# Kernel optimization log

Hardware: AMD Instinct MI355X
Metric: run time of the kernel (lower is better)

The kernel has to match this reference:

```python
import jax, jax.numpy as jnp
import numpy as np

N_QUBITS = 8
DEPTH = 6
BATCH = 32
C = jnp.complex64

# Noise strengths from get_ibm_noise_params: constants derived from IBM Nairobi gate errors.
G1, G2 = 0.0003, 0.0065

def _amp_kraus(g):
    return [jnp.array([[1.0, 0.0], [0.0, np.sqrt(1.0 - g)]], C),
            jnp.array([[0.0, np.sqrt(g)], [0.0, 0.0]], C)]

def _phase_kraus(g):
    return [jnp.array([[1.0, 0.0], [0.0, np.sqrt(1.0 - g)]], C),
            jnp.array([[0.0, 0.0], [0.0, np.sqrt(g)]], C)]

def _depol_kraus(p):
    s0, s = np.sqrt(1.0 - p), np.sqrt(p / 3.0)
    I = np.eye(2); X = np.array([[0, 1], [1, 0]])
    Y = np.array([[0, -1j], [1j, 0]]); Z = np.diag([1, -1])
    return [jnp.array(s0 * I, C), jnp.array(s * X, C), jnp.array(s * Y, C), jnp.array(s * Z, C)]

# channels applied sequentially: amplitude damping, phase damping, depolarizing
CH_1Q = [_amp_kraus(G1 * 0.3), _phase_kraus(G1 * 0.2), _depol_kraus(G1 * 0.5)]
CH_2Q = [_amp_kraus(G2 * 0.3), _phase_kraus(G2 * 0.2), _depol_kraus(G2 * 0.5)]

CNOT4 = jnp.array([[1, 0, 0, 0], [0, 1, 0, 0], [0, 0, 0, 1], [0, 0, 1, 0]], C).reshape(2, 2, 2, 2)

# rho is a per-sample tensor of shape (2,)*(2*N): axes [0..N) are row indices, [N..2N) col indices.

def apply_1q(rho, U, w):
    # rho -> U rho U^dagger on wire w
    rho = jnp.moveaxis(jnp.tensordot(U, rho, axes=([1], [w])), 0, w)
    return jnp.moveaxis(jnp.tensordot(jnp.conj(U), rho, axes=([1], [N_QUBITS + w])), 0, N_QUBITS + w)

def apply_channel(rho, kraus, w):
    out = apply_1q(rho, kraus[0], w)
    for K in kraus[1:]:
        out = out + apply_1q(rho, K, w)
    return out

def apply_noise(rho, channels, w):
    for kraus in channels:
        rho = apply_channel(rho, kraus, w)
    return rho

def apply_cnot(rho, w):
    rho = jnp.moveaxis(jnp.tensordot(CNOT4, rho, axes=([2, 3], [w, w + 1])), [0, 1], [w, w + 1])
    return jnp.moveaxis(jnp.tensordot(jnp.conj(CNOT4), rho,
                                      axes=([2, 3], [N_QUBITS + w, N_QUBITS + w + 1])),
                        [0, 1], [N_QUBITS + w, N_QUBITS + w + 1])

def ry(t):
    c, s = jnp.cos(t / 2), jnp.sin(t / 2)
    return jnp.stack([jnp.stack([c, -s]), jnp.stack([s, c])]).astype(C)

def rz(t):
    em = jnp.exp(-0.5j * t).astype(C)  # exp(-i t/2)
    zero = jnp.zeros((), C)
    return jnp.stack([jnp.stack([em, zero]), jnp.stack([zero, jnp.conj(em)])])

def circuit(x, weights):
    # x: [N_QUBITS] angles; weights: [DEPTH, N_QUBITS, 2]
    shape = (2,) * (2 * N_QUBITS)
    rho = jnp.zeros(shape, C).at[(0,) * (2 * N_QUBITS)].set(1.0)

    def encode(rho, x):
        for i in range(N_QUBITS):
            rho = apply_1q(rho, ry(x[i]), i)
            rho = apply_noise(rho, CH_1Q, i)
        return rho

    rho = jax.checkpoint(encode)(rho, x)

    def layer(rho, wl):
        for i in range(N_QUBITS - 1):
            rho = apply_cnot(rho, i)
            rho = apply_noise(rho, CH_2Q, i)
            rho = apply_noise(rho, CH_2Q, i + 1)
        for i in range(N_QUBITS):
            rho = apply_1q(rho, ry(wl[i, 0]), i)
            rho = apply_1q(rho, rz(wl[i, 1]), i)
            rho = apply_noise(rho, CH_1Q, i)
        return rho, None

    rho, _ = jax.lax.scan(jax.checkpoint(layer), rho, weights)

    D = 2 ** N_QUBITS
    diag = jnp.diagonal(rho.reshape(D, D))
    # PauliZ on wire 0 (most significant bit in PennyLane ordering): +1 first half, -1 second half
    sign = jnp.where(jnp.arange(D) < D // 2, 1.0, -1.0)
    return jnp.real(jnp.sum(diag * sign)).astype(jnp.float32)


def setup_inputs() -> dict:
    key = jax.random.key(0)
    k1, k2 = jax.random.split(key)
    x = jax.random.normal(k1, (BATCH, N_QUBITS), dtype=jnp.float32)
    weights = jax.random.normal(k2, (DEPTH, N_QUBITS, 2), dtype=jnp.float32) * 0.1
    return {"x": x, "weights": weights}


def reference(x, weights):
    out = jax.vmap(circuit, in_axes=(0, None))(x, weights)  # [B]
    return out[:, None]  # [B, 1], matches torch .unsqueeze(1)
```

## Files before the change

### kernel.cpp

```cpp
#include <hip/hip_runtime.h>
#include <cmath>


typedef float2 cplx;
#define BATCH 32

__device__ __forceinline__ cplx cmul(cplx a, cplx b){
  return make_float2(a.x*b.x - a.y*b.y, a.x*b.y + a.y*b.x);
}
__device__ __forceinline__ cplx lc(float a, cplx u, float b, cplx v){
  return make_float2(a*u.x + b*v.x, a*u.y + b*v.y);
}
__device__ __forceinline__ cplx sc(float a, cplx u){ return make_float2(a*u.x, a*u.y); }

struct N1C { float A,B,C,D,E; };
__device__ __forceinline__ N1C noise_coeffs(float g){
  float ga = g*0.3f, gp = g*0.2f, p = g*0.5f;
  N1C n;
  n.A = 1.0f - 2.0f*p/3.0f;
  n.D = 2.0f*p/3.0f;
  n.B = ga*n.A + n.D*(1.0f-ga);
  n.E = n.D*ga + n.A*(1.0f-ga);
  n.C = (1.0f - 4.0f*p/3.0f) * sqrtf(1.0f-ga) * sqrtf(1.0f-gp);
  return n;
}
__device__ __forceinline__ N1C mkadj(N1C n){
  N1C a; a.A=n.A; a.B=n.D; a.C=n.C; a.D=n.B; a.E=n.E; return a;
}

__device__ __forceinline__ int physof(int L){
  int rl = L >> 6;
  int rot = ((rl<<3)|(rl>>3)) & 63;
  return L ^ rot;
}
__device__ __forceinline__ constexpr int KPc(int p){
  return (p < 6) ? (1<<p) : ((1<<p) | (1 << ((p-3)%6)));
}
__device__ __forceinline__ int physB(int L){
  int rl = L >> 5;
  int rot = ((rl<<2)|(rl>>3)) & 31;
  return L ^ rot;
}
__device__ __forceinline__ constexpr int maskB(int p){
  return (p < 5) ? (1<<p) : ((1<<p) | (1 << ((p-3)%5)));
}

template<int U>
__device__ __forceinline__ int baseF(int g){
  constexpr int F[6][8] = {
    {0,0,0,0,0,0,0,0},
    {2,4,9, 3,5,8,10,11},
    {0,3,5, 4,6,9,10,11},
    {0,1,4, 5,6,7,10,11},
    {1,2,5, 0,6,7,8,11},
    {0,2,3, 1,6,7,8,9}};
  int b = 0;
  #pragma unroll
  for (int i=0;i<8;i++) b ^= (-((g>>i)&1)) & KPc(F[U][i]);
  return b;
}
template<int V>
__device__ __forceinline__ int baseBk(int g){
  constexpr int F[5][6] = {
    {0,0,0,0,0,0},
    {3,4, 2,7,8,9},
    {0,4, 3,5,8,9},
    {0,1, 4,5,6,9},
    {1,2, 0,5,6,7}};
  int b = 0;
  #pragma unroll
  for (int i=0;i<6;i++) b ^= (-((g>>i)&1)) & maskB(F[V][i]);
  return b;
}
__device__ __forceinline__ int base_s(int t){
  constexpr int P[10] = {1,2,3,9, 4,5,7,8,10,11};
  int b = 0;
  #pragma unroll
  for (int i=0;i<10;i++) b ^= (-((t>>i)&1)) & KPc(P[i]);
  return b;
}

__device__ __forceinline__ void rot_pair(cplx& v0, cplx& v1, float cy, float sy){
  cplx a=v0, b=v1;
  v0 = make_float2(cy*a.x - sy*b.x, cy*a.y - sy*b.y);
  v1 = make_float2(sy*a.x + cy*b.x, sy*a.y + cy*b.y);
}

template<int U>
__device__ __forceinline__ void fstage2(cplx* __restrict__ slab, float4 rc, int bp, int bsel,
                                        N1C n1, N1C n2, float a0, float b0, float a1, float b1){
  constexpr int KA=KPc(6+U), KB=KPc(5+U), KC=1<<U, KD=1<<(U-1);
  cplx h[8];
  #pragma unroll
  for (int i=0;i<8;i++){
    int a=(i>>2)&1, cc=(i>>1)&1, d=i&1;
    h[i] = slab[bp ^ (a?KA:0) ^ ((bsel^a)?KB:0) ^ (cc?KC:0) ^ ((d^cc)?KD:0)];
  }
  #pragma unroll
  for (int d=0;d<2;d++){
    cplx t00=h[d], t11=h[6|d];
    h[d]   = lc(n2.A,t00, n2.B,t11);
    h[6|d] = lc(n2.D,t00, n2.E,t11);
    h[2|d] = sc(n2.C, h[2|d]);
    h[4|d] = sc(n2.C, h[4|d]);
  }
  #pragma unroll
  for (int j=0;j<4;j++){
    int i0 = j<<1;
    float r0x = __shfl_xor(h[i0].x, 1, 64),   r0y = __shfl_xor(h[i0].y, 1, 64);
    float r1x = __shfl_xor(h[i0|1].x, 1, 64), r1y = __shfl_xor(h[i0|1].y, 1, 64);
    cplx h0 = h[i0], h1 = h[i0|1];
    h[i0]   = make_float2(a0*h0.x + b0*r1x, a0*h0.y + b0*r1y);
    h[i0|1] = make_float2(a1*h1.x + b1*r0x, a1*h1.y + b1*r0y);
  }
  float cy=rc.x, sy=rc.y;
  #pragma unroll
  for (int a=0;a<2;a++)
    #pragma unroll
    for (int d=0;d<2;d++) rot_pair(h[(a<<2)|d], h[(a<<2)|2|d], cy, sy);
  #pragma unroll
  for (int cc=0;cc<2;cc++)
    #pragma unroll
    for (int d=0;d<2;d++) rot_pair(h[(cc<<1)|d], h[4|(cc<<1)|d], cy, sy);
  cplx p = make_float2(rc.z, rc.w), pcj = make_float2(rc.z, -rc.w);
  #pragma unroll
  for (int d=0;d<2;d++){
    cplx t00=h[d], t11=h[6|d];
    h[d]   = lc(n1.A,t00, n1.B,t11);
    h[6|d] = lc(n1.D,t00, n1.E,t11);
    h[2|d] = cmul(p,   h[2|d]);
    h[4|d] = cmul(pcj, h[4|d]);
  }
  #pragma unroll
  for (int i=0;i<8;i++){
    int a=(i>>2)&1, cc=(i>>1)&1, d=i&1;
    slab[bp ^ (a?KA:0) ^ (bsel?KB:0) ^ (cc?KC:0) ^ (d?KD:0)] = h[i];
  }
}

__device__ __forceinline__ void redT50(cplx* __restrict__ slab, float4 rc, float g6,
                                       N1C n1, N1C n2, int t){
  constexpr int KR = KPc(6), KCb = 1;
  #pragma unroll
  for (int grp=0; grp<2; grp++){
    int bp = base_s(t | (grp<<9));
    cplx v00 = slab[bp], v01 = slab[bp^KCb], v10 = slab[bp^KR], v11 = slab[bp^KR^KCb];
    v01 = sc(g6, v01); v10 = sc(g6, v10);
    { cplx t00=v00, t11=v11;
      v00 = lc(n2.A,t00, n2.B,t11); v11 = lc(n2.D,t00, n2.E,t11);
      v01 = sc(n2.C,v01); v10 = sc(n2.C,v10); }
    float cy=rc.x, sy=rc.y;
    rot_pair(v00,v01,cy,sy); rot_pair(v10,v11,cy,sy);
    rot_pair(v00,v10,cy,sy); rot_pair(v01,v11,cy,sy);
    { cplx t00=v00, t11=v11;
      v00 = lc(n1.A,t00, n1.B,t11); v11 = lc(n1.D,t00, n1.E,t11);
      v01 = cmul(make_float2(rc.z,rc.w),  v01);
      v10 = cmul(make_float2(rc.z,-rc.w), v10); }
    slab[bp] = v00; slab[bp^KCb] = v01; slab[bp^KR] = v10; slab[bp^KR^KCb] = v11;
  }
}

template<int V>
__device__ __forceinline__ void astage_q4b(cplx* __restrict__ slab, float4 rc, int bp,
                                           int bsel, int dsel, N1C n1a, N1C n2a,
                                           float alpha, float beta){
  constexpr int KA=maskB(5+V), KB=maskB(4+V), KC=1<<V, KD=1<<(V-1);
  int fix = (bsel?KB:0) ^ (dsel?KD:0);
  cplx v[4];
  v[0] = slab[bp ^ fix];
  v[1] = slab[bp ^ fix ^ KC];
  v[2] = slab[bp ^ fix ^ KA];
  v[3] = slab[bp ^ fix ^ KA ^ KC];
  cplx p  = make_float2(rc.z, -rc.w);
  cplx pc = make_float2(rc.z,  rc.w);
  float cy=rc.x, sy=-rc.y;
  {
    cplx t00=v[0], t11=v[3];
    v[0]=lc(n1a.A,t00, n1a.B,t11);
    v[3]=lc(n1a.D,t00, n1a.E,t11);
    v[1]=cmul(p,v[1]); v[2]=cmul(pc,v[2]);
    rot_pair(v[0],v[1],cy,sy); rot_pair(v[2],v[3],cy,sy);
    rot_pair(v[0],v[2],cy,sy); rot_pair(v[1],v[3],cy,sy);
  }
  #pragma unroll
  for (int j=0;j<4;j++){
    float rx = __shfl_xor(v[j].x, 3, 64);
    float ry = __shfl_xor(v[j].y, 3, 64);
    v[j] = make_float2(alpha*v[j].x + beta*rx, alpha*v[j].y + beta*ry);
  }
  {
    cplx t00=v[0], t11=v[3];
    v[0]=lc(n2a.A,t00, n2a.B,t11);
    v[3]=lc(n2a.D,t00, n2a.E,t11);
    v[1]=sc(n2a.C,v[1]); v[2]=sc(n2a.C,v[2]);
  }
  int sb = bsel ? KB : 0;
  slab[bp ^ sb            ^ (dsel?KD:0)]      = v[0];
  slab[bp ^ sb ^ KC       ^ (dsel?0:KD)]      = v[1];
  slab[bp ^ (sb^KB) ^ KA  ^ (dsel?KD:0)]      = v[2];
  slab[bp ^ (sb^KB) ^ KA ^ KC ^ (dsel?0:KD)]  = v[3];
}

#define SLOT2(UU, FI, VV, BI) { \
  if (t < 512) fstage2<UU>(fslab, sS[FI], baseF<UU>(gf), bf, n1, n2, a0,b0,a1,b1); \
  else if (t < 768) astage_q4b<VV>(bslab, sS[BI], baseBk<VV>(gb), bb_, db_, n1a, n2a, alpha, beta); \
  __syncthreads(); }

__global__ __launch_bounds__(1024) void fused_kernel(const float* __restrict__ x,
                                                     const float* __restrict__ w,
                                                     float* __restrict__ out){
  __shared__ cplx fslab[4096];
  __shared__ cplx bslab[1024];
  __shared__ float4 sS[48];
  __shared__ float sm[28];
  __shared__ float red[16];
  int t = threadIdx.x, s = blockIdx.x;
  N1C n1 = noise_coeffs(0.0003f);
  N1C n2 = noise_coeffs(0.0065f);
  N1C n1a = mkadj(n1), n2a = mkadj(n2);
  int bf = t & 1, gf = t >> 1;
  float a0 = bf ? n2.C : n2.A;
  float b0 = bf ? 0.f  : n2.B;
  float a1 = bf ? n2.E : n2.C;
  float b1 = bf ? n2.D : 0.f;
  int db_ = t & 1, bb_ = (t >> 1) & 1, gb = (t >> 2) & 63;
  float alpha = (bb_==db_) ? (bb_ ? n2a.E : n2a.A) : n2a.C;
  float beta  = (bb_==db_) ? (bb_ ? n2a.D : n2a.B) : 0.f;

  if (t < 48){
    float w0=w[t*2], w1=w[t*2+1];
    sS[t] = make_float4(cosf(0.5f*w0), sinf(0.5f*w0), n1.C*cosf(w1), -n1.C*sinf(w1));
  }
  if (t < 7){
    float xv = x[s*8+t];
    float c = cosf(0.5f*xv), sn = sinf(0.5f*xv);
    float p00=c*c, p01=c*sn, p11=sn*sn;
    sm[t*4+0]=n1.A*p00+n1.B*p11; sm[t*4+1]=n1.C*p01;
    sm[t*4+2]=n1.C*p01;          sm[t*4+3]=n1.D*p00+n1.E*p11;
  }
  __syncthreads();
  #pragma unroll
  for (int k=0;k<4;k++){
    int L = k*1024 + t, rl = L>>6, cl = L&63;
    float v = 1.f;
    #pragma unroll
    for (int q=0;q<6;q++)
      v *= sm[q*4 + ((rl>>(5-q))&1)*2 + ((cl>>(5-q))&1)];
    fslab[physof(L)] = make_float2(v, 0.f);
  }
  if (t >= 512 && t < 768){
    int local = t - 512;
    #pragma unroll
    for (int k=0;k<4;k++){
      int o = k*256 + local, r = o>>5, c = o&31;
      bslab[physB(o)] = make_float2((r==c) ? ((r&16)? -1.f : 1.f) : 0.f, 0.f);
    }
  }
  float g6 = 2.f * sm[25];
  __syncthreads();

  SLOT2(5, 0, 4, 40)
  SLOT2(4, 1, 3, 33)
  SLOT2(3, 2, 4, 32)
  SLOT2(2, 3, 2, 26)
  SLOT2(1, 4, 3, 25)
  {
    if (t < 512) redT50(fslab, sS[5], g6, n1, n2, t);
    else if (t < 768) astage_q4b<4>(bslab, sS[24], baseBk<4>(gb), bb_, db_, n1a, n2a, alpha, beta);
    __syncthreads();
  }
  SLOT2(5, 8, 1, 19)
  SLOT2(4, 9, 2, 18)
  SLOT2(3,10, 3, 17)
  SLOT2(2,11, 4, 16)
  {
    if (t < 512) fstage2<1>(fslab, sS[12], baseF<1>(gf), bf, n1, n2, a0,b0,a1,b1);
    __syncthreads();
  }

  float acc;
  {
    int r04 = t >> 5, c04 = t & 31;
    cplx Ov = bslab[physB(t)];
    cplx z = make_float2(0.f,0.f);
    #pragma unroll
    for (int b5=0;b5<2;b5++){
      int L = ((((c04<<1)|b5)<<6) | ((r04<<1)|b5));
      cplx rv = fslab[physof(L)];
      z = make_float2(z.x+rv.x, z.y+rv.y);
    }
    acc = Ov.x*z.x - Ov.y*z.y;
  }
  #pragma unroll
  for (int off=32; off>0; off>>=1) acc += __shfl_down(acc, off, 64);
  if ((t&63)==0) red[t>>6] = acc;
  __syncthreads();
  if (t==0){
    float v = 0.f;
    #pragma unroll
    for (int k=0;k<16;k++) v += red[k];
    out[s] = v;
  }
}

extern "C" void kernel_launch(void* const* d_in, const int* in_sizes, int n_in,
                              void* d_out, int out_size, void* d_ws, size_t ws_size,
                              hipStream_t stream) {
  const float* x = (const float*)d_in[0];
  const float* w = (const float*)d_in[1];
  float* out = (float*)d_out;

  fused_kernel<<<BATCH, 1024, 0, stream>>>(x, w, out);
}
```

Measured before the change: 22.38 us.

## Fold final forward stage into readout contraction and use DPP for lane swaps

```diff
diff --git a/kernel.cpp b/kernel.cpp
--- a/kernel.cpp
+++ b/kernel.cpp
@@ -8,6 +8,7 @@
 __device__ __forceinline__ cplx cmul(cplx a, cplx b){
   return make_float2(a.x*b.x - a.y*b.y, a.x*b.y + a.y*b.x);
 }
+__device__ __forceinline__ cplx cadd(cplx a, cplx b){ return make_float2(a.x+b.x, a.y+b.y); }
 __device__ __forceinline__ cplx lc(float a, cplx u, float b, cplx v){
   return make_float2(a*u.x + b*v.x, a*u.y + b*v.y);
 }
@@ -28,6 +29,13 @@
   N1C a; a.A=n.A; a.B=n.D; a.C=n.C; a.D=n.B; a.E=n.E; return a;
 }
 
+__device__ __forceinline__ float dpp_x1(float v){
+  return __int_as_float(__builtin_amdgcn_mov_dpp(__float_as_int(v), 0xB1, 0xF, 0xF, true));
+}
+__device__ __forceinline__ float dpp_x3(float v){
+  return __int_as_float(__builtin_amdgcn_mov_dpp(__float_as_int(v), 0x1B, 0xF, 0xF, true));
+}
+
 __device__ __forceinline__ int physof(int L){
   int rl = L >> 6;
   int rot = ((rl<<3)|(rl>>3)) & 63;
@@ -107,8 +115,8 @@
   #pragma unroll
   for (int j=0;j<4;j++){
     int i0 = j<<1;
-    float r0x = __shfl_xor(h[i0].x, 1, 64),   r0y = __shfl_xor(h[i0].y, 1, 64);
-    float r1x = __shfl_xor(h[i0|1].x, 1, 64), r1y = __shfl_xor(h[i0|1].y, 1, 64);
+    float r0x = dpp_x1(h[i0].x),   r0y = dpp_x1(h[i0].y);
+    float r1x = dpp_x1(h[i0|1].x), r1y = dpp_x1(h[i0|1].y);
     cplx h0 = h[i0], h1 = h[i0|1];
     h[i0]   = make_float2(a0*h0.x + b0*r1x, a0*h0.y + b0*r1y);
     h[i0|1] = make_float2(a1*h1.x + b1*r0x, a1*h1.y + b1*r0y);
@@ -184,8 +192,8 @@
   }
   #pragma unroll
   for (int j=0;j<4;j++){
-    float rx = __shfl_xor(v[j].x, 3, 64);
-    float ry = __shfl_xor(v[j].y, 3, 64);
+    float rx = dpp_x3(v[j].x);
+    float ry = dpp_x3(v[j].y);
     v[j] = make_float2(alpha*v[j].x + beta*rx, alpha*v[j].y + beta*ry);
   }
   {
@@ -213,6 +221,7 @@
   __shared__ cplx bslab[1024];
   __shared__ float4 sS[48];
   __shared__ float sm[28];
+  __shared__ cplx C4s[16];
   __shared__ float red[16];
   int t = threadIdx.x, s = blockIdx.x;
   N1C n1 = noise_coeffs(0.0003f);
@@ -238,6 +247,32 @@
     sm[t*4+0]=n1.A*p00+n1.B*p11; sm[t*4+1]=n1.C*p01;
     sm[t*4+2]=n1.C*p01;          sm[t*4+3]=n1.D*p00+n1.E*p11;
   }
+  if (t == 63){
+    float w0=w[24], w1=w[25];
+    float c = cosf(0.5f*w0), sn = sinf(0.5f*w0);
+    float U[2][2] = {{c,-sn},{sn,c}};
+    cplx ph01 = make_float2(cosf(w1), -sinf(w1));
+    cplx ph10 = make_float2(ph01.x, -ph01.y);
+    cplx S4[16];
+    #pragma unroll
+    for (int a=0;a<2;a++)
+      #pragma unroll
+      for (int b=0;b<2;b++){
+        int k = 2*a+b;
+        float u0a=U[0][a], u0b=U[0][b], u1a=U[1][a], u1b=U[1][b];
+        S4[0*4+k] = make_float2(n1.A*u0a*u0b + n1.B*u1a*u1b, 0.f);
+        S4[1*4+k] = sc(n1.C*u0a*u1b, ph01);
+        S4[2*4+k] = sc(n1.C*u1a*u0b, ph10);
+        S4[3*4+k] = make_float2(n1.D*u0a*u0b + n1.E*u1a*u1b, 0.f);
+      }
+    #pragma unroll
+    for (int j=0;j<4;j++){
+      C4s[j*4+0] = cadd(sc(n2.A, S4[j*4+0]), sc(n2.D, S4[j*4+3]));
+      C4s[j*4+1] = sc(n2.C, S4[j*4+1]);
+      C4s[j*4+2] = sc(n2.C, S4[j*4+2]);
+      C4s[j*4+3] = cadd(sc(n2.B, S4[j*4+0]), sc(n2.E, S4[j*4+3]));
+    }
+  }
   __syncthreads();
   #pragma unroll
   for (int k=0;k<4;k++){
@@ -273,22 +308,24 @@
   SLOT2(4, 9, 2, 18)
   SLOT2(3,10, 3, 17)
   SLOT2(2,11, 4, 16)
-  {
-    if (t < 512) fstage2<1>(fslab, sS[12], baseF<1>(gf), bf, n1, n2, a0,b0,a1,b1);
-    __syncthreads();
-  }
 
   float acc;
   {
     int r04 = t >> 5, c04 = t & 31;
+    int r03 = r04 >> 1, r4 = r04 & 1, c03 = c04 >> 1, c4 = c04 & 1;
+    int rbase = c03 << 2, cbase = r03 << 2;
+    #define FEL(al,be,ga,de) fslab[physof((((rbase|((al)<<1)|(be))<<6) | (cbase|((ga)<<1)|(de))))]
+    cplx Q0 = cadd(FEL(0,0,0,0), FEL(0,1,0,1));
+    cplx Q1 = cadd(FEL(0,0,1,1), FEL(0,1,1,0));
+    cplx Q2 = cadd(FEL(1,1,0,0), FEL(1,0,0,1));
+    cplx Q3 = cadd(FEL(1,1,1,1), FEL(1,0,1,0));
+    #undef FEL
+    int j = ((c4<<1)|r4) << 2;
+    cplx z = cmul(C4s[j], Q0);
+    z = cadd(z, cmul(C4s[j|1], Q1));
+    z = cadd(z, cmul(C4s[j|2], Q2));
+    z = cadd(z, cmul(C4s[j|3], Q3));
     cplx Ov = bslab[physB(t)];
-    cplx z = make_float2(0.f,0.f);
-    #pragma unroll
-    for (int b5=0;b5<2;b5++){
-      int L = ((((c04<<1)|b5)<<6) | ((r04<<1)|b5));
-      cplx rv = fslab[physof(L)];
-      z = make_float2(z.x+rv.x, z.y+rv.y);
-    }
     acc = Ov.x*z.x - Ov.y*z.y;
   }
   #pragma unroll
```

After: 20.11 us. -10.1%, faster.
